# Performance work log

Hardware: AMD Instinct MI355X
Metric: run time of the kernel (lower is better)

## Reference

```python
import jax, jax.numpy as jnp
import numpy as np

N_NODES = 50000

# DGL ChebConv with k=2 and the standard lambda_max=2 approximation:
#   L_hat = L - I = -D^{-1/2} A D^{-1/2}
#   X0 = X ; X1 = L_hat @ X ; out = concat([X0, X1], -1) @ W + b
# Norm uses in-degrees (DGL behavior).

def setup_inputs() -> dict:
    key = jax.random.key(0)
    ks = jax.random.split(key, 8)
    E = 800000
    src = jax.random.randint(ks[0], (E,), 0, N_NODES, dtype=jnp.int32)
    dst = jax.random.randint(ks[1], (E,), 0, N_NODES, dtype=jnp.int32)
    def w(k, shape):
        fan_in = shape[0]
        return jax.random.normal(k, shape, jnp.float32) * (1.0 / np.sqrt(fan_in))
    return {
        "x": jax.random.normal(ks[2], (N_NODES, 128), jnp.float32),
        "src": src, "dst": dst,
        "W1": w(ks[3], (256, 256)), "b1": jnp.zeros((256,), jnp.float32),
        "W2": w(ks[4], (512, 256)), "b2": jnp.zeros((256,), jnp.float32),
        "W3": w(ks[5], (512, 128)), "b3": jnp.zeros((128,), jnp.float32),
    }

def _cheb_layer(h, src, dst, dinv, W, b):
    # X1 = -D^{-1/2} A D^{-1/2} h  (lambda_max = 2)
    hn = h * dinv[:, None]
    agg = jax.ops.segment_sum(hn[src], dst, num_segments=N_NODES)
    x1 = -(agg * dinv[:, None])
    return jnp.concatenate([h, x1], axis=-1) @ W + b

def reference(x, src, dst, W1, b1, W2, b2, W3, b3):
    deg = jax.ops.segment_sum(jnp.ones_like(dst, dtype=x.dtype), dst,
                              num_segments=N_NODES)
    dinv = jnp.where(deg > 0, jax.lax.rsqrt(jnp.maximum(deg, 1.0)), 0.0)
    h = jnp.tanh(_cheb_layer(x, src, dst, dinv, W1, b1))
    for _ in range(3):  # hid_layer = 3
        h = jnp.tanh(_cheb_layer(h, src, dst, dinv, W2, b2))
    return _cheb_layer(h, src, dst, dinv, W3, b3)
```

## Files before the change

kernel.cpp:

```cpp
#include <hip/hip_runtime.h>
#include <cmath>

#define NN 50000
#define CAP 64

typedef short v8s __attribute__((ext_vector_type(8)));
typedef float v4f __attribute__((ext_vector_type(4)));

__device__ __forceinline__ float b2f(unsigned short u) {
    return __uint_as_float(((unsigned int)u) << 16);
}
__device__ __forceinline__ unsigned short f2b(float f) {
    unsigned int x = __float_as_uint(f);
    x += 0x7fffu + ((x >> 16) & 1u);
    return (unsigned short)(x >> 16);
}

__device__ __forceinline__ void gld16(const void* g, void* l) {
    __builtin_amdgcn_global_load_lds(
        (const __attribute__((address_space(1))) unsigned int*)g,
        (__attribute__((address_space(3))) unsigned int*)l, 16, 0, 0);
}

__global__ void sniff_kernel(const unsigned short* __restrict__ x, int* __restrict__ mode) {
    if (threadIdx.x == 0 && blockIdx.x == 0) {
        int c = 0;
        for (int i = 0; i < 128; ++i) {
            unsigned int e = (x[i] >> 7) & 0xFFu;
            if (e >= 100u && e <= 140u) ++c;
        }
        *mode = (c >= 112) ? 0 : 1;
    }
}

__global__ void fill_kernel(const int* __restrict__ src, const int* __restrict__ dst,
                            int* __restrict__ cnt, unsigned short* __restrict__ ell, int E) {
    int e = blockIdx.x * blockDim.x + threadIdx.x;
    if (e < E) {
        int d = dst[e];
        int pos = atomicAdd(&cnt[d], 1);
        if (pos < CAP) ell[d * CAP + pos] = (unsigned short)src[e];
    }
}

__global__ void dinv_kernel(const int* __restrict__ cnt, float* __restrict__ dinv, int n) {
    int i = blockIdx.x * blockDim.x + threadIdx.x;
    if (i < n) {
        int d = cnt[i];
        dinv[i] = (d > 0) ? rsqrtf((float)d) : 0.0f;
    }
}

__global__ void prep_kernel(const void* __restrict__ x,
                            const void* __restrict__ W1, const void* __restrict__ W2,
                            const void* __restrict__ W3, const void* __restrict__ b1,
                            const void* __restrict__ b2, const void* __restrict__ b3,
                            unsigned short* __restrict__ buf,
                            unsigned short* __restrict__ WT1, unsigned short* __restrict__ WT2,
                            unsigned short* __restrict__ WT3, unsigned short* __restrict__ bb1,
                            unsigned short* __restrict__ bb2, unsigned short* __restrict__ bb3,
                            const int* __restrict__ modep) {
    int mode = *modep;
    int b = blockIdx.x, t = threadIdx.x;
    if (b < 3125) {
        int idx = b * 256 + t;
        int n = idx >> 4, c = idx & 15;
        if (mode == 0) {
            ((uint4*)buf)[n * 64 + c] = ((const uint4*)x)[idx];
        } else {
            const float* xf = (const float*)x + (size_t)idx * 8;
            unsigned short o[8];
#pragma unroll
            for (int i = 0; i < 8; ++i) o[i] = f2b(xf[i]);
            ((uint4*)buf)[n * 64 + c] = *(const uint4*)o;
        }
    } else if (b < 3381) {
        int idx = (b - 3125) * 256 + t;
        int n = idx >> 8, k = idx & 255;
        WT1[idx] = mode ? f2b(((const float*)W1)[k * 256 + n])
                        : ((const unsigned short*)W1)[k * 256 + n];
    } else if (b < 3893) {
        int idx = (b - 3381) * 256 + t;
        int n = idx >> 9, k = idx & 511;
        WT2[idx] = mode ? f2b(((const float*)W2)[k * 256 + n])
                        : ((const unsigned short*)W2)[k * 256 + n];
    } else if (b < 4149) {
        int idx = (b - 3893) * 256 + t;
        int n = idx >> 9, k = idx & 511;
        WT3[idx] = mode ? f2b(((const float*)W3)[k * 128 + n])
                        : ((const unsigned short*)W3)[k * 128 + n];
    } else {
        if (t < 256) {
            bb1[t] = mode ? f2b(((const float*)b1)[t]) : ((const unsigned short*)b1)[t];
            bb2[t] = mode ? f2b(((const float*)b2)[t]) : ((const unsigned short*)b2)[t];
        }
        if (t < 128)
            bb3[t] = mode ? f2b(((const float*)b3)[t]) : ((const unsigned short*)b3)[t];
    }
}

template <int FPL>
__global__ void spmm_kernel(const unsigned short* __restrict__ h, int ldh,
                            const int* __restrict__ cnt, const unsigned short* __restrict__ ell,
                            const float* __restrict__ dinv,
                            unsigned short* __restrict__ out, int ldo) {
    int node = blockIdx.x * 4 + (threadIdx.x >> 6);
    int lane = threadIdx.x & 63;
    int c = cnt[node]; c = (c < CAP) ? c : CAP;
    int sl = (int)ell[node * CAP + lane];
    float dl = dinv[sl];
    float acc[FPL];
#pragma unroll
    for (int i = 0; i < FPL; ++i) acc[i] = 0.f;
    const int col = lane * FPL;

    int g = 0;
    for (; g + 8 <= c; g += 8) {
        int s[8]; float d[8];
#pragma unroll
        for (int i = 0; i < 8; ++i) { s[i] = __shfl(sl, g + i); d[i] = __shfl(dl, g + i); }
        if (FPL == 4) {
            ushort4 v[8];
#pragma unroll
            for (int i = 0; i < 8; ++i)
                v[i] = *(const ushort4*)(h + (size_t)s[i] * ldh + col);
#pragma unroll
            for (int i = 0; i < 8; ++i) {
                acc[0] += d[i] * b2f(v[i].x); acc[1] += d[i] * b2f(v[i].y);
                acc[2] += d[i] * b2f(v[i].z); acc[3] += d[i] * b2f(v[i].w);
            }
        } else {
            ushort2 v[8];
#pragma unroll
            for (int i = 0; i < 8; ++i)
                v[i] = *(const ushort2*)(h + (size_t)s[i] * ldh + col);
#pragma unroll
            for (int i = 0; i < 8; ++i) {
                acc[0] += d[i] * b2f(v[i].x); acc[1] += d[i] * b2f(v[i].y);
            }
        }
    }
    for (; g < c; ++g) {
        int sg = __shfl(sl, g);
        float dg = __shfl(dl, g);
        const unsigned short* hp = h + (size_t)sg * ldh + col;
        if (FPL == 4) {
            ushort4 v = *(const ushort4*)hp;
            acc[0] += dg * b2f(v.x); acc[1] += dg * b2f(v.y);
            acc[2] += dg * b2f(v.z); acc[3] += dg * b2f(v.w);
        } else {
            ushort2 v = *(const ushort2*)hp;
            acc[0] += dg * b2f(v.x); acc[1] += dg * b2f(v.y);
        }
    }

    float dn = -dinv[node];
    unsigned short* op = out + (size_t)node * ldo + col;
    if (FPL == 4) {
        ushort4 o;
        o.x = f2b(acc[0] * dn); o.y = f2b(acc[1] * dn);
        o.z = f2b(acc[2] * dn); o.w = f2b(acc[3] * dn);
        *(ushort4*)op = o;
    } else {
        ushort2 o;
        o.x = f2b(acc[0] * dn); o.y = f2b(acc[1] * dn);
        *(ushort2*)op = o;
    }
}

template <int K32, int NQ>
__global__ void __launch_bounds__(2 * NQ * 64)
gemm_lds_kernel(const unsigned short* __restrict__ A, int lda,
                const unsigned short* __restrict__ WT,
                const unsigned short* __restrict__ bias,
                void* __restrict__ out, int ldo,
                int M, int dotanh, int is_final, const int* __restrict__ modep) {
    constexpr int K    = K32 * 32;
    constexpr int NB   = NQ * 64;
    constexpr int NTHR = 2 * NQ * 64;
    constexpr int ACH  = 128 * 4;
    constexpr int BCH  = NB * 4;
    constexpr int ROUNDS = (ACH + BCH) / NTHR;
    constexpr int LDSZ  = (128 + NB) * 32;
    __shared__ unsigned short lds[2 * LDSZ];

    const int tid = threadIdx.x;
    const int wave = tid >> 6, lane = tid & 63, quad = lane >> 4, l16 = lane & 15;
    const int mh = wave / NQ, nq = wave % NQ;
    const int m0 = blockIdx.x * 128;

    v4f acc[4][4];
#pragma unroll
    for (int mi = 0; mi < 4; ++mi)
#pragma unroll
        for (int ni = 0; ni < 4; ++ni) acc[mi][ni] = (v4f){0.f, 0.f, 0.f, 0.f};

    const unsigned short* gp[ROUNDS];
#pragma unroll
    for (int r = 0; r < ROUNDS; ++r) {
        int c = tid + r * NTHR;
        if (c < ACH) {
            int row = m0 + (c >> 2);
            if (row >= M) row = M - 1;
            gp[r] = A + (size_t)row * lda + (c & 3) * 8;
        } else {
            int cb = c - ACH;
            gp[r] = WT + (size_t)(cb >> 2) * K + (cb & 3) * 8;
        }
    }

    auto STAGE = [&](int bsel, int k0) {
#pragma unroll
        for (int r = 0; r < ROUNDS; ++r) {
            int c = tid + r * NTHR;
            gld16(gp[r] + k0, (void*)&lds[bsel * LDSZ + c * 8]);
        }
    };

    STAGE(0, 0);
#pragma unroll 1
    for (int t = 0; t < K32; ++t) {
        if (t + 1 < K32) {
            STAGE((t + 1) & 1, (t + 1) * 32);
            asm volatile("s_waitcnt vmcnt(%0)" :: "i"(ROUNDS) : "memory");
        } else {
            asm volatile("s_waitcnt vmcnt(0)" ::: "memory");
        }
        __builtin_amdgcn_s_barrier();

        const unsigned short* aT = &lds[(t & 1) * LDSZ];
        const unsigned short* bT = aT + 128 * 32;
        v8s a_frag[4], b_frag[4];
#pragma unroll
        for (int mi = 0; mi < 4; ++mi)
            a_frag[mi] = *(const v8s*)&aT[(mh * 64 + mi * 16 + l16) * 32 + quad * 8];
#pragma unroll
        for (int ni = 0; ni < 4; ++ni)
            b_frag[ni] = *(const v8s*)&bT[(nq * 64 + ni * 16 + l16) * 32 + quad * 8];
#pragma unroll
        for (int mi = 0; mi < 4; ++mi)
#pragma unroll
            for (int ni = 0; ni < 4; ++ni)
                acc[mi][ni] = __builtin_amdgcn_mfma_f32_16x16x32_bf16(a_frag[mi], b_frag[ni],
                                                                      acc[mi][ni], 0, 0, 0);
        asm volatile("s_waitcnt lgkmcnt(0)" ::: "memory");
        __builtin_amdgcn_s_barrier();
    }

    int fin = is_final ? *modep : 0;
#pragma unroll
    for (int ni = 0; ni < 4; ++ni) {
        int colc = nq * 64 + ni * 16 + l16;
        float bv = b2f(bias[colc]);
#pragma unroll
        for (int mi = 0; mi < 4; ++mi) {
#pragma unroll
            for (int r = 0; r < 4; ++r) {
                int row = m0 + mh * 64 + mi * 16 + quad * 4 + r;
                if (row < M) {
                    float v = acc[mi][ni][r] + bv;
                    if (dotanh) v = tanhf(v);
                    if (fin) ((float*)out)[(size_t)row * ldo + colc] = v;
                    else     ((unsigned short*)out)[(size_t)row * ldo + colc] = f2b(v);
                }
            }
        }
    }
}

static inline size_t al256(size_t x) { return (x + 255) & ~(size_t)255; }

extern "C" void kernel_launch(void* const* d_in, const int* in_sizes, int n_in,
                              void* d_out, int out_size, void* d_ws, size_t ws_size,
                              hipStream_t stream) {
    const void* x  = d_in[0];
    const int* src = (const int*)d_in[1];
    const int* dst = (const int*)d_in[2];
    const void* W1 = d_in[3]; const void* b1 = d_in[4];
    const void* W2 = d_in[5]; const void* b2 = d_in[6];
    const void* W3 = d_in[7]; const void* b3 = d_in[8];
    const int E = in_sizes[1];

    char* p = (char*)d_ws;
    int* mode     = (int*)p;            p += 256;
    int* cnt      = (int*)p;            p += al256((size_t)NN * 4);
    float* dinv   = (float*)p;          p += al256((size_t)NN * 4);
    unsigned short* ell = (unsigned short*)p; p += al256((size_t)NN * CAP * 2);
    unsigned short* WT1 = (unsigned short*)p; p += al256((size_t)256 * 256 * 2);
    unsigned short* WT2 = (unsigned short*)p; p += al256((size_t)256 * 512 * 2);
    unsigned short* WT3 = (unsigned short*)p; p += al256((size_t)128 * 512 * 2);
    unsigned short* bb1 = (unsigned short*)p; p += al256((size_t)256 * 2);
    unsigned short* bb2 = (unsigned short*)p; p += al256((size_t)256 * 2);
    unsigned short* bb3 = (unsigned short*)p; p += al256((size_t)128 * 2);
    unsigned short* buf = (unsigned short*)p; p += al256((size_t)NN * 512 * 2);

    hipMemsetAsync(cnt, 0, (size_t)NN * 4, stream);
    sniff_kernel<<<1, 64, 0, stream>>>((const unsigned short*)x, mode);
    prep_kernel<<<4150, 256, 0, stream>>>(x, W1, W2, W3, b1, b2, b3,
                                          buf, WT1, WT2, WT3, bb1, bb2, bb3, mode);
    int eb = (E + 255) / 256;
    fill_kernel<<<eb, 256, 0, stream>>>(src, dst, cnt, ell, E);
    dinv_kernel<<<(NN + 255) / 256, 256, 0, stream>>>(cnt, dinv, NN);

    const int SPMM_GRID = NN / 4;
    const int GB = (NN + 127) / 128;

    spmm_kernel<2><<<SPMM_GRID, 256, 0, stream>>>(buf, 512, cnt, ell, dinv, buf + 128, 512);
    gemm_lds_kernel<8, 4><<<GB, 512, 0, stream>>>(buf, 512, WT1, bb1, buf, 512, NN, 1, 0, mode);
    spmm_kernel<4><<<SPMM_GRID, 256, 0, stream>>>(buf, 512, cnt, ell, dinv, buf + 256, 512);
    gemm_lds_kernel<16, 4><<<GB, 512, 0, stream>>>(buf, 512, WT2, bb2, buf, 512, NN, 1, 0, mode);
    spmm_kernel<4><<<SPMM_GRID, 256, 0, stream>>>(buf, 512, cnt, ell, dinv, buf + 256, 512);
    gemm_lds_kernel<16, 4><<<GB, 512, 0, stream>>>(buf, 512, WT2, bb2, buf, 512, NN, 1, 0, mode);
    spmm_kernel<4><<<SPMM_GRID, 256, 0, stream>>>(buf, 512, cnt, ell, dinv, buf + 256, 512);
    gemm_lds_kernel<16, 4><<<GB, 512, 0, stream>>>(buf, 512, WT2, bb2, buf, 512, NN, 1, 0, mode);
    spmm_kernel<4><<<SPMM_GRID, 256, 0, stream>>>(buf, 512, cnt, ell, dinv, buf + 256, 512);
    gemm_lds_kernel<16, 2><<<GB, 256, 0, stream>>>(buf, 512, WT3, bb3, d_out, 128, NN, 0, 1, mode);
}
```

Baseline: 545.7 us.

## Reorder final layer to aggregate after projection and shrink GEMM tile to 64 rows

The last Chebyshev layer now projects h with the lower half of W3 first, giving 128 columns, and runs the sparse aggregation on that narrower result. The final GEMM then adds the aggregated term in its epilogue, which halves the gather width of the last SpMM. All GEMMs move to a 64-row tile with one wave per 64 output columns, giving more blocks and smaller LDS use but less reuse of each loaded weight tile. The bf16 rounding of the intermediate projection changes numerics slightly, and the sniff kernel is parallelised with a ballot.

```diff
diff --git a/kernel.cpp b/kernel.cpp
--- a/kernel.cpp
+++ b/kernel.cpp
@@ -23,14 +23,13 @@
 }
 
 __global__ void sniff_kernel(const unsigned short* __restrict__ x, int* __restrict__ mode) {
-    if (threadIdx.x == 0 && blockIdx.x == 0) {
-        int c = 0;
-        for (int i = 0; i < 128; ++i) {
-            unsigned int e = (x[i] >> 7) & 0xFFu;
-            if (e >= 100u && e <= 140u) ++c;
-        }
-        *mode = (c >= 112) ? 0 : 1;
-    }
+    __shared__ int c2[2];
+    int t = threadIdx.x;
+    unsigned int e = (x[t] >> 7) & 0xFFu;
+    unsigned long long m = __ballot(e >= 100u && e <= 140u);
+    if ((t & 63) == 0) c2[t >> 6] = __popcll(m);
+    __syncthreads();
+    if (t == 0) *mode = (c2[0] + c2[1] >= 112) ? 0 : 1;
 }
 
 __global__ void fill_kernel(const int* __restrict__ src, const int* __restrict__ dst,
@@ -59,6 +58,7 @@
                             unsigned short* __restrict__ WT1, unsigned short* __restrict__ WT2,
                             unsigned short* __restrict__ WT3, unsigned short* __restrict__ bb1,
                             unsigned short* __restrict__ bb2, unsigned short* __restrict__ bb3,
+                            unsigned short* __restrict__ bbz,
                             const int* __restrict__ modep) {
     int mode = *modep;
     int b = blockIdx.x, t = threadIdx.x;
@@ -94,8 +94,10 @@
             bb1[t] = mode ? f2b(((const float*)b1)[t]) : ((const unsigned short*)b1)[t];
             bb2[t] = mode ? f2b(((const float*)b2)[t]) : ((const unsigned short*)b2)[t];
         }
-        if (t < 128)
+        if (t < 128) {
             bb3[t] = mode ? f2b(((const float*)b3)[t]) : ((const unsigned short*)b3)[t];
+            bbz[t] = 0;
+        }
     }
 }
 
@@ -169,25 +171,25 @@
 }
 
 template <int K32, int NQ>
-__global__ void __launch_bounds__(2 * NQ * 64)
-gemm_lds_kernel(const unsigned short* __restrict__ A, int lda,
-                const unsigned short* __restrict__ WT,
-                const unsigned short* __restrict__ bias,
-                void* __restrict__ out, int ldo,
-                int M, int dotanh, int is_final, const int* __restrict__ modep) {
-    constexpr int K    = K32 * 32;
+__global__ void __launch_bounds__(NQ * 64)
+gemm64_kernel(const unsigned short* __restrict__ A, int lda,
+              const unsigned short* __restrict__ WT, int ldw, int kw0,
+              const unsigned short* __restrict__ bias,
+              const unsigned short* __restrict__ addv, int ldav,
+              void* __restrict__ out, int ldo,
+              int M, int dotanh, int is_final, const int* __restrict__ modep) {
     constexpr int NB   = NQ * 64;
-    constexpr int NTHR = 2 * NQ * 64;
-    constexpr int ACH  = 128 * 4;
+    constexpr int NTHR = NQ * 64;
+    constexpr int ACH  = 64 * 4;
     constexpr int BCH  = NB * 4;
     constexpr int ROUNDS = (ACH + BCH) / NTHR;
-    constexpr int LDSZ  = (128 + NB) * 32;
+    constexpr int LDSZ  = (64 + NB) * 32;
     __shared__ unsigned short lds[2 * LDSZ];
 
     const int tid = threadIdx.x;
-    const int wave = tid >> 6, lane = tid & 63, quad = lane >> 4, l16 = lane & 15;
-    const int mh = wave / NQ, nq = wave % NQ;
-    const int m0 = blockIdx.x * 128;
+    const int lane = tid & 63, quad = lane >> 4, l16 = lane & 15;
+    const int nq = tid >> 6;
+    const int m0 = blockIdx.x * 64;
 
     v4f acc[4][4];
 #pragma unroll
@@ -205,7 +207,7 @@
             gp[r] = A + (size_t)row * lda + (c & 3) * 8;
         } else {
             int cb = c - ACH;
-            gp[r] = WT + (size_t)(cb >> 2) * K + (cb & 3) * 8;
+            gp[r] = WT + (size_t)(cb >> 2) * ldw + kw0 + (cb & 3) * 8;
         }
     }
 
@@ -229,11 +231,11 @@
         __builtin_amdgcn_s_barrier();
 
         const unsigned short* aT = &lds[(t & 1) * LDSZ];
-        const unsigned short* bT = aT + 128 * 32;
+        const unsigned short* bT = aT + 64 * 32;
         v8s a_frag[4], b_frag[4];
 #pragma unroll
         for (int mi = 0; mi < 4; ++mi)
-            a_frag[mi] = *(const v8s*)&aT[(mh * 64 + mi * 16 + l16) * 32 + quad * 8];
+            a_frag[mi] = *(const v8s*)&aT[(mi * 16 + l16) * 32 + quad * 8];
 #pragma unroll
         for (int ni = 0; ni < 4; ++ni)
             b_frag[ni] = *(const v8s*)&bT[(nq * 64 + ni * 16 + l16) * 32 + quad * 8];
@@ -256,9 +258,10 @@
         for (int mi = 0; mi < 4; ++mi) {
 #pragma unroll
             for (int r = 0; r < 4; ++r) {
-                int row = m0 + mh * 64 + mi * 16 + quad * 4 + r;
+                int row = m0 + mi * 16 + quad * 4 + r;
                 if (row < M) {
                     float v = acc[mi][ni][r] + bv;
+                    if (addv) v += b2f(addv[(size_t)row * ldav + colc]);
                     if (dotanh) v = tanhf(v);
                     if (fin) ((float*)out)[(size_t)row * ldo + colc] = v;
                     else     ((unsigned short*)out)[(size_t)row * ldo + colc] = f2b(v);
@@ -292,27 +295,36 @@
     unsigned short* bb1 = (unsigned short*)p; p += al256((size_t)256 * 2);
     unsigned short* bb2 = (unsigned short*)p; p += al256((size_t)256 * 2);
     unsigned short* bb3 = (unsigned short*)p; p += al256((size_t)128 * 2);
+    unsigned short* bbz = (unsigned short*)p; p += al256((size_t)128 * 2);
     unsigned short* buf = (unsigned short*)p; p += al256((size_t)NN * 512 * 2);
 
     hipMemsetAsync(cnt, 0, (size_t)NN * 4, stream);
-    sniff_kernel<<<1, 64, 0, stream>>>((const unsigned short*)x, mode);
+    sniff_kernel<<<1, 128, 0, stream>>>((const unsigned short*)x, mode);
     prep_kernel<<<4150, 256, 0, stream>>>(x, W1, W2, W3, b1, b2, b3,
-                                          buf, WT1, WT2, WT3, bb1, bb2, bb3, mode);
+                                          buf, WT1, WT2, WT3, bb1, bb2, bb3, bbz, mode);
     int eb = (E + 255) / 256;
     fill_kernel<<<eb, 256, 0, stream>>>(src, dst, cnt, ell, E);
     dinv_kernel<<<(NN + 255) / 256, 256, 0, stream>>>(cnt, dinv, NN);
 
     const int SPMM_GRID = NN / 4;
-    const int GB = (NN + 127) / 128;
+    const int GB = (NN + 63) / 64;
 
     spmm_kernel<2><<<SPMM_GRID, 256, 0, stream>>>(buf, 512, cnt, ell, dinv, buf + 128, 512);
-    gemm_lds_kernel<8, 4><<<GB, 512, 0, stream>>>(buf, 512, WT1, bb1, buf, 512, NN, 1, 0, mode);
+    gemm64_kernel<8, 4><<<GB, 256, 0, stream>>>(buf, 512, WT1, 256, 0, bb1,
+                                                nullptr, 0, buf, 512, NN, 1, 0, mode);
     spmm_kernel<4><<<SPMM_GRID, 256, 0, stream>>>(buf, 512, cnt, ell, dinv, buf + 256, 512);
-    gemm_lds_kernel<16, 4><<<GB, 512, 0, stream>>>(buf, 512, WT2, bb2, buf, 512, NN, 1, 0, mode);
+    gemm64_kernel<16, 4><<<GB, 256, 0, stream>>>(buf, 512, WT2, 512, 0, bb2,
+                                                 nullptr, 0, buf, 512, NN, 1, 0, mode);
     spmm_kernel<4><<<SPMM_GRID, 256, 0, stream>>>(buf, 512, cnt, ell, dinv, buf + 256, 512);
-    gemm_lds_kernel<16, 4><<<GB, 512, 0, stream>>>(buf, 512, WT2, bb2, buf, 512, NN, 1, 0, mode);
+    gemm64_kernel<16, 4><<<GB, 256, 0, stream>>>(buf, 512, WT2, 512, 0, bb2,
+                                                 nullptr, 0, buf, 512, NN, 1, 0, mode);
     spmm_kernel<4><<<SPMM_GRID, 256, 0, stream>>>(buf, 512, cnt, ell, dinv, buf + 256, 512);
-    gemm_lds_kernel<16, 4><<<GB, 512, 0, stream>>>(buf, 512, WT2, bb2, buf, 512, NN, 1, 0, mode);
-    spmm_kernel<4><<<SPMM_GRID, 256, 0, stream>>>(buf, 512, cnt, ell, dinv, buf + 256, 512);
-    gemm_lds_kernel<16, 2><<<GB, 256, 0, stream>>>(buf, 512, WT3, bb3, d_out, 128, NN, 0, 1, mode);
-}
+    gemm64_kernel<16, 4><<<GB, 256, 0, stream>>>(buf, 512, WT2, 512, 0, bb2,
+                                                 nullptr, 0, buf, 512, NN, 1, 0, mode);
+    gemm64_kernel<8, 2><<<GB, 128, 0, stream>>>(buf, 512, WT3, 512, 256, bbz,
+                                                nullptr, 0, buf + 256, 512, NN, 0, 0, mode);
+    spmm_kernel<2><<<SPMM_GRID, 256, 0, stream>>>(buf + 256, 512, cnt, ell, dinv,
+                                                  buf + 384, 512);
+    gemm64_kernel<8, 2><<<GB, 128, 0, stream>>>(buf, 512, WT3, 512, 0, bb3,
+                                                buf + 384, 512, d_out, 128, NN, 0, 1, mode);
+}
```

Result: slower. 605.9 us (+11.0%).

## Triple-buffer GEMM LDS staging, XOR-swizzle LDS layout, parallelize sniff kernel

Applied to the files above, without the earlier changes.

The GEMM now uses three LDS buffers with a prefetch distance of two K-tiles and issues the next stage right after the barrier, which removes the trailing barrier in each iteration. LDS tile columns are XOR-swizzled by row to cut bank conflicts on the fragment reads. The single-thread sniff loop becomes a 128-thread ballot/popcount reduction. In exchange, LDS use per block goes up by half, which may lower occupancy.

```diff
diff --git a/kernel.cpp b/kernel.cpp
--- a/kernel.cpp
+++ b/kernel.cpp
@@ -23,14 +23,13 @@
 }
 
 __global__ void sniff_kernel(const unsigned short* __restrict__ x, int* __restrict__ mode) {
-    if (threadIdx.x == 0 && blockIdx.x == 0) {
-        int c = 0;
-        for (int i = 0; i < 128; ++i) {
-            unsigned int e = (x[i] >> 7) & 0xFFu;
-            if (e >= 100u && e <= 140u) ++c;
-        }
-        *mode = (c >= 112) ? 0 : 1;
-    }
+    __shared__ int c2[2];
+    int t = threadIdx.x;
+    unsigned int e = (x[t] >> 7) & 0xFFu;
+    unsigned long long m = __ballot(e >= 100u && e <= 140u);
+    if ((t & 63) == 0) c2[t >> 6] = __popcll(m);
+    __syncthreads();
+    if (t == 0) *mode = (c2[0] + c2[1] >= 112) ? 0 : 1;
 }
 
 __global__ void fill_kernel(const int* __restrict__ src, const int* __restrict__ dst,
@@ -182,7 +181,7 @@
     constexpr int BCH  = NB * 4;
     constexpr int ROUNDS = (ACH + BCH) / NTHR;
     constexpr int LDSZ  = (128 + NB) * 32;
-    __shared__ unsigned short lds[2 * LDSZ];
+    __shared__ unsigned short lds[3 * LDSZ];
 
     const int tid = threadIdx.x;
     const int wave = tid >> 6, lane = tid & 63, quad = lane >> 4, l16 = lane & 15;
@@ -200,12 +199,16 @@
     for (int r = 0; r < ROUNDS; ++r) {
         int c = tid + r * NTHR;
         if (c < ACH) {
-            int row = m0 + (c >> 2);
-            if (row >= M) row = M - 1;
-            gp[r] = A + (size_t)row * lda + (c & 3) * 8;
+            int row = c >> 2;
+            int quadg = (c & 3) ^ ((row >> 1) & 3);
+            int grow = m0 + row;
+            if (grow >= M) grow = M - 1;
+            gp[r] = A + (size_t)grow * lda + quadg * 8;
         } else {
             int cb = c - ACH;
-            gp[r] = WT + (size_t)(cb >> 2) * K + (cb & 3) * 8;
+            int row = cb >> 2;
+            int quadg = (cb & 3) ^ ((row >> 1) & 3);
+            gp[r] = WT + (size_t)row * K + quadg * 8;
         }
     }
 
@@ -218,25 +221,29 @@
     };
 
     STAGE(0, 0);
+    if (K32 > 1) STAGE(1, 32);
+
+    const int q8 = (quad ^ ((l16 >> 1) & 3)) * 8;
+
 #pragma unroll 1
     for (int t = 0; t < K32; ++t) {
         if (t + 1 < K32) {
-            STAGE((t + 1) & 1, (t + 1) * 32);
             asm volatile("s_waitcnt vmcnt(%0)" :: "i"(ROUNDS) : "memory");
         } else {
             asm volatile("s_waitcnt vmcnt(0)" ::: "memory");
         }
         __builtin_amdgcn_s_barrier();
-
-        const unsigned short* aT = &lds[(t & 1) * LDSZ];
+        if (t + 2 < K32) STAGE((t + 2) % 3, (t + 2) * 32);
+
+        const unsigned short* aT = &lds[(t % 3) * LDSZ];
         const unsigned short* bT = aT + 128 * 32;
         v8s a_frag[4], b_frag[4];
 #pragma unroll
         for (int mi = 0; mi < 4; ++mi)
-            a_frag[mi] = *(const v8s*)&aT[(mh * 64 + mi * 16 + l16) * 32 + quad * 8];
+            a_frag[mi] = *(const v8s*)&aT[(mh * 64 + mi * 16 + l16) * 32 + q8];
 #pragma unroll
         for (int ni = 0; ni < 4; ++ni)
-            b_frag[ni] = *(const v8s*)&bT[(nq * 64 + ni * 16 + l16) * 32 + quad * 8];
+            b_frag[ni] = *(const v8s*)&bT[(nq * 64 + ni * 16 + l16) * 32 + q8];
 #pragma unroll
         for (int mi = 0; mi < 4; ++mi)
 #pragma unroll
@@ -244,7 +251,6 @@
                 acc[mi][ni] = __builtin_amdgcn_mfma_f32_16x16x32_bf16(a_frag[mi], b_frag[ni],
                                                                       acc[mi][ni], 0, 0, 0);
         asm volatile("s_waitcnt lgkmcnt(0)" ::: "memory");
-        __builtin_amdgcn_s_barrier();
     }
 
     int fin = is_final ? *modep : 0;
@@ -295,7 +301,7 @@
     unsigned short* buf = (unsigned short*)p; p += al256((size_t)NN * 512 * 2);
 
     hipMemsetAsync(cnt, 0, (size_t)NN * 4, stream);
-    sniff_kernel<<<1, 64, 0, stream>>>((const unsigned short*)x, mode);
+    sniff_kernel<<<1, 128, 0, stream>>>((const unsigned short*)x, mode);
     prep_kernel<<<4150, 256, 0, stream>>>(x, W1, W2, W3, b1, b2, b3,
                                           buf, WT1, WT2, WT3, bb1, bb2, bb3, mode);
     int eb = (E + 255) / 256;
```

After: 603.7 us. 10.6% more time.

## Reassociate final layer to project before aggregation, halving last SpMM width

Applied to the files above, without the earlier changes.

The last layer now multiplies h by the lower half of W3 first (a 256-to-128 projection), aggregates that narrower 128-wide result with the SpMM, and then runs the upper-half GEMM with the aggregated term added in its epilogue. This uses linearity, (L h) W = L (h W), so the final sparse gather moves 128 features per edge instead of 256. In exchange it adds an extra GEMM launch and more epilogue reads, and rounding the intermediate to bf16 before aggregation may shift numerics slightly. The sniff kernel is also changed to use a wave ballot across 128 threads instead of a serial loop.

```diff
diff --git a/kernel.cpp b/kernel.cpp
--- a/kernel.cpp
+++ b/kernel.cpp
@@ -23,14 +23,13 @@
 }
 
 __global__ void sniff_kernel(const unsigned short* __restrict__ x, int* __restrict__ mode) {
-    if (threadIdx.x == 0 && blockIdx.x == 0) {
-        int c = 0;
-        for (int i = 0; i < 128; ++i) {
-            unsigned int e = (x[i] >> 7) & 0xFFu;
-            if (e >= 100u && e <= 140u) ++c;
-        }
-        *mode = (c >= 112) ? 0 : 1;
-    }
+    __shared__ int c2[2];
+    int t = threadIdx.x;
+    unsigned int e = (x[t] >> 7) & 0xFFu;
+    unsigned long long m = __ballot(e >= 100u && e <= 140u);
+    if ((t & 63) == 0) c2[t >> 6] = __popcll(m);
+    __syncthreads();
+    if (t == 0) *mode = (c2[0] + c2[1] >= 112) ? 0 : 1;
 }
 
 __global__ void fill_kernel(const int* __restrict__ src, const int* __restrict__ dst,
@@ -59,6 +58,7 @@
                             unsigned short* __restrict__ WT1, unsigned short* __restrict__ WT2,
                             unsigned short* __restrict__ WT3, unsigned short* __restrict__ bb1,
                             unsigned short* __restrict__ bb2, unsigned short* __restrict__ bb3,
+                            unsigned short* __restrict__ bbz,
                             const int* __restrict__ modep) {
     int mode = *modep;
     int b = blockIdx.x, t = threadIdx.x;
@@ -94,8 +94,10 @@
             bb1[t] = mode ? f2b(((const float*)b1)[t]) : ((const unsigned short*)b1)[t];
             bb2[t] = mode ? f2b(((const float*)b2)[t]) : ((const unsigned short*)b2)[t];
         }
-        if (t < 128)
+        if (t < 128) {
             bb3[t] = mode ? f2b(((const float*)b3)[t]) : ((const unsigned short*)b3)[t];
+            bbz[t] = 0;
+        }
     }
 }
 
@@ -168,14 +170,14 @@
     }
 }
 
-template <int K32, int NQ>
+template <int K32, int NQ, int LDW, int KW0, bool ADDV>
 __global__ void __launch_bounds__(2 * NQ * 64)
 gemm_lds_kernel(const unsigned short* __restrict__ A, int lda,
                 const unsigned short* __restrict__ WT,
                 const unsigned short* __restrict__ bias,
+                const unsigned short* __restrict__ addv, int ldav,
                 void* __restrict__ out, int ldo,
                 int M, int dotanh, int is_final, const int* __restrict__ modep) {
-    constexpr int K    = K32 * 32;
     constexpr int NB   = NQ * 64;
     constexpr int NTHR = 2 * NQ * 64;
     constexpr int ACH  = 128 * 4;
@@ -205,7 +207,7 @@
             gp[r] = A + (size_t)row * lda + (c & 3) * 8;
         } else {
             int cb = c - ACH;
-            gp[r] = WT + (size_t)(cb >> 2) * K + (cb & 3) * 8;
+            gp[r] = WT + (size_t)(cb >> 2) * LDW + KW0 + (cb & 3) * 8;
         }
     }
 
@@ -259,6 +261,7 @@
                 int row = m0 + mh * 64 + mi * 16 + quad * 4 + r;
                 if (row < M) {
                     float v = acc[mi][ni][r] + bv;
+                    if constexpr (ADDV) v += b2f(addv[(size_t)row * ldav + colc]);
                     if (dotanh) v = tanhf(v);
                     if (fin) ((float*)out)[(size_t)row * ldo + colc] = v;
                     else     ((unsigned short*)out)[(size_t)row * ldo + colc] = f2b(v);
@@ -292,12 +295,13 @@
     unsigned short* bb1 = (unsigned short*)p; p += al256((size_t)256 * 2);
     unsigned short* bb2 = (unsigned short*)p; p += al256((size_t)256 * 2);
     unsigned short* bb3 = (unsigned short*)p; p += al256((size_t)128 * 2);
+    unsigned short* bbz = (unsigned short*)p; p += al256((size_t)128 * 2);
     unsigned short* buf = (unsigned short*)p; p += al256((size_t)NN * 512 * 2);
 
     hipMemsetAsync(cnt, 0, (size_t)NN * 4, stream);
-    sniff_kernel<<<1, 64, 0, stream>>>((const unsigned short*)x, mode);
+    sniff_kernel<<<1, 128, 0, stream>>>((const unsigned short*)x, mode);
     prep_kernel<<<4150, 256, 0, stream>>>(x, W1, W2, W3, b1, b2, b3,
-                                          buf, WT1, WT2, WT3, bb1, bb2, bb3, mode);
+                                          buf, WT1, WT2, WT3, bb1, bb2, bb3, bbz, mode);
     int eb = (E + 255) / 256;
     fill_kernel<<<eb, 256, 0, stream>>>(src, dst, cnt, ell, E);
     dinv_kernel<<<(NN + 255) / 256, 256, 0, stream>>>(cnt, dinv, NN);
@@ -306,13 +310,21 @@
     const int GB = (NN + 127) / 128;
 
     spmm_kernel<2><<<SPMM_GRID, 256, 0, stream>>>(buf, 512, cnt, ell, dinv, buf + 128, 512);
-    gemm_lds_kernel<8, 4><<<GB, 512, 0, stream>>>(buf, 512, WT1, bb1, buf, 512, NN, 1, 0, mode);
+    gemm_lds_kernel<8, 4, 256, 0, false><<<GB, 512, 0, stream>>>(
+        buf, 512, WT1, bb1, nullptr, 0, buf, 512, NN, 1, 0, mode);
     spmm_kernel<4><<<SPMM_GRID, 256, 0, stream>>>(buf, 512, cnt, ell, dinv, buf + 256, 512);
-    gemm_lds_kernel<16, 4><<<GB, 512, 0, stream>>>(buf, 512, WT2, bb2, buf, 512, NN, 1, 0, mode);
+    gemm_lds_kernel<16, 4, 512, 0, false><<<GB, 512, 0, stream>>>(
+        buf, 512, WT2, bb2, nullptr, 0, buf, 512, NN, 1, 0, mode);
     spmm_kernel<4><<<SPMM_GRID, 256, 0, stream>>>(buf, 512, cnt, ell, dinv, buf + 256, 512);
-    gemm_lds_kernel<16, 4><<<GB, 512, 0, stream>>>(buf, 512, WT2, bb2, buf, 512, NN, 1, 0, mode);
+    gemm_lds_kernel<16, 4, 512, 0, false><<<GB, 512, 0, stream>>>(
+        buf, 512, WT2, bb2, nullptr, 0, buf, 512, NN, 1, 0, mode);
     spmm_kernel<4><<<SPMM_GRID, 256, 0, stream>>>(buf, 512, cnt, ell, dinv, buf + 256, 512);
-    gemm_lds_kernel<16, 4><<<GB, 512, 0, stream>>>(buf, 512, WT2, bb2, buf, 512, NN, 1, 0, mode);
-    spmm_kernel<4><<<SPMM_GRID, 256, 0, stream>>>(buf, 512, cnt, ell, dinv, buf + 256, 512);
-    gemm_lds_kernel<16, 2><<<GB, 256, 0, stream>>>(buf, 512, WT3, bb3, d_out, 128, NN, 0, 1, mode);
-}
+    gemm_lds_kernel<16, 4, 512, 0, false><<<GB, 512, 0, stream>>>(
+        buf, 512, WT2, bb2, nullptr, 0, buf, 512, NN, 1, 0, mode);
+    gemm_lds_kernel<8, 2, 512, 256, false><<<GB, 256, 0, stream>>>(
+        buf, 512, WT3, bbz, nullptr, 0, buf + 256, 512, NN, 0, 0, mode);
+    spmm_kernel<2><<<SPMM_GRID, 256, 0, stream>>>(buf + 256, 512, cnt, ell, dinv,
+                                                  buf + 384, 512);
+    gemm_lds_kernel<8, 2, 512, 0, true><<<GB, 256, 0, stream>>>(
+        buf, 512, WT3, bb3, buf + 384, 512, d_out, 128, NN, 0, 1, mode);
+}
```

Result: no change. 540.3 us (median of 2 runs) (-1.0%).
